# Optimization experiments

Measured on AMD Instinct MI355X. Metric: run time of the kernel, lower is better.

## Reference

```python
import jax, jax.numpy as jnp
import numpy as np

B, T = 64, 200
NUM_C2 = 2000
NUM_D = 1000
V = 128

# NOTE: Dropout layers are identity in eval mode; this reference implements eval-mode forward.

def setup_inputs() -> dict:
    key = jax.random.key(0)
    ks = jax.random.split(key, 19)
    s = 0.05
    def nrm(k, shape):
        return jax.random.normal(k, shape, jnp.float32) * s
    return {
        "c_seq": jax.random.randint(ks[0], (B, T), 0, NUM_C2),
        "d_seq": jax.random.randint(ks[1], (B, T), 0, NUM_D),
        "r_seq": (jax.random.uniform(ks[2], (B, T)) < 0.5).astype(jnp.float32),
        "D_emb": nrm(ks[3], (NUM_D, 1)),
        "v_d": nrm(ks[4], (V,)),
        "v_r": nrm(ks[5], (V,)),
        "v_c": nrm(ks[6], (V,)),
        "W_ih": nrm(ks[7], (3 * V, 2 * V)),
        "W_hh": nrm(ks[8], (3 * V, V)),
        "b_ih": nrm(ks[9], (3 * V,)),
        "b_hh": nrm(ks[10], (3 * V,)),
        "W1a": nrm(ks[11], (V, V)),
        "b1a": nrm(ks[12], (V,)),
        "W1b": nrm(ks[13], (1, V)),
        "b1b": nrm(ks[14], (1,)),
        "W2a": nrm(ks[15], (V, 3 * V)),
        "b2a": nrm(ks[16], (V,)),
        "W2b": nrm(ks[17], (1, V)),
        "b2b": nrm(ks[18], (1,)),
    }


def reference(c_seq, d_seq, r_seq, D_emb, v_d, v_r, v_c,
              W_ih, W_hh, b_ih, b_hh, W1a, b1a, W1b, b1b,
              W2a, b2a, W2b, b2b):
    gamma_seq = D_emb[d_seq]                 # [B,T,1]
    v_d_seq = gamma_seq * v_d                # [B,T,V]
    v_r_seq = r_seq[..., None] * v_r         # [B,T,V]
    x = jnp.concatenate([v_d_seq, v_r_seq], axis=-1)  # [B,T,2V]

    # --- GRU (PyTorch gate ordering r,z,n), h0 = 0 ---
    def gru_step(h, x_t):
        gi = x_t @ W_ih.T + b_ih
        gh = h @ W_hh.T + b_hh
        i_r, i_z, i_n = jnp.split(gi, 3, axis=-1)
        h_r, h_z, h_n = jnp.split(gh, 3, axis=-1)
        r = jax.nn.sigmoid(i_r + h_r)
        z = jax.nn.sigmoid(i_z + h_z)
        n = jnp.tanh(i_n + r * h_n)
        h_new = (1.0 - z) * n + z * h
        return h_new, h_new

    h0 = jnp.zeros((c_seq.shape[0], v_d.shape[0]), x.dtype)
    _, h_seq = jax.lax.scan(gru_step, h0, jnp.swapaxes(x, 0, 1))
    h_seq = jnp.swapaxes(h_seq, 0, 1)        # [B,T,V]

    # linear_1 (dropout = identity in eval)
    alpha_seq = (jax.nn.relu(h_seq @ W1a.T + b1a) @ W1b.T + b1b)[..., 0]  # [B,T]

    # --- sequential memory update over time ---
    def mem_step(C, inputs):
        c_t, vd_t, vr_t = inputs             # [B], [B,V], [B,V]
        beta = jnp.take_along_axis(C, c_t[:, None], axis=1)   # [B,1]
        vc = beta * v_c                       # [B,V]
        hh = jax.nn.relu(jnp.concatenate([vc, vd_t, vr_t], axis=-1) @ W2a.T + b2a)
        new_c = hh @ W2b.T + b2b              # [B,1]
        oh = jax.nn.one_hot(c_t, C.shape[1], dtype=C.dtype)   # [B,K]
        C_new = C * (1.0 - oh) + new_c * oh
        return C_new, C_new

    C0 = jnp.zeros((c_seq.shape[0], NUM_C2), x.dtype)
    _, C_seq = jax.lax.scan(
        mem_step, C0,
        (jnp.swapaxes(c_seq, 0, 1), jnp.swapaxes(v_d_seq, 0, 1), jnp.swapaxes(v_r_seq, 0, 1)))
    C_seq = jnp.swapaxes(C_seq, 0, 1)[..., None]   # [B,T,K,1]
    return alpha_seq, h_seq, C_seq
```

## Files before the change

### kernel.cpp

```cpp
#include <hip/hip_runtime.h>
#include <hip/hip_bf16.h>
#include <cstdint>

#define BB 64
#define TT 200
#define KN 2000
#define VV 128
#define NGRU 16

typedef __attribute__((ext_vector_type(8))) short bf16x8;
typedef __attribute__((ext_vector_type(4))) float f32x4;
typedef _Float16 half8 __attribute__((ext_vector_type(8)));


__device__ __forceinline__ float sigm(float x) {
    return __builtin_amdgcn_rcpf(1.f + __expf(-x));
}
__device__ __forceinline__ float tanh_f(float x) {
    float e = __expf(2.f * x);
    return 1.f - 2.f * __builtin_amdgcn_rcpf(e + 1.f);
}

__device__ __forceinline__ void soft_barrier() {
    asm volatile("s_waitcnt lgkmcnt(0)" ::: "memory");
    __builtin_amdgcn_s_barrier();
    __builtin_amdgcn_sched_barrier(0);
}

__global__ void pre_kernel(const float* __restrict__ v_d, const float* __restrict__ v_r,
                           const float* __restrict__ v_c, const float* __restrict__ W_ih,
                           const float* __restrict__ W2a, float* __restrict__ ws)
{
    int g = blockIdx.x * 256 + threadIdx.x;
    float* pd = ws;
    float* pr = ws + 384;
    float* uc = ws + 768;
    float* ud = ws + 896;
    float* ur = ws + 1024;
    if (g < 384) {
        float a = 0.f, b = 0.f;
        for (int k = 0; k < VV; ++k) {
            a = fmaf(W_ih[g * 256 + k], v_d[k], a);
            b = fmaf(W_ih[g * 256 + VV + k], v_r[k], b);
        }
        pd[g] = a; pr[g] = b;
    }
    if (g < VV) {
        float a = 0.f, b = 0.f, c = 0.f;
        for (int k = 0; k < VV; ++k) {
            a = fmaf(W2a[g * 384 + k], v_c[k], a);
            b = fmaf(W2a[g * 384 + VV + k], v_d[k], b);
            c = fmaf(W2a[g * 384 + 2 * VV + k], v_r[k], c);
        }
        uc[g] = a; ud[g] = b; ur[g] = c;
    }
}

__device__ __forceinline__ half8 load_cvt8h(const float* p) {
    float4 a = *(const float4*)p;
    float4 c = *(const float4*)(p + 4);
    half8 r;
    r[0] = (_Float16)a.x; r[1] = (_Float16)a.y; r[2] = (_Float16)a.z; r[3] = (_Float16)a.w;
    r[4] = (_Float16)c.x; r[5] = (_Float16)c.y; r[6] = (_Float16)c.z; r[7] = (_Float16)c.w;
    return r;
}

__global__ __launch_bounds__(512, 1) void fused_kernel(
    const int* __restrict__ c_seq, const int* __restrict__ d_seq,
    const float* __restrict__ r_seq, const float* __restrict__ D_emb,
    const float* __restrict__ Whh, const float* __restrict__ bih,
    const float* __restrict__ bhh, const float* __restrict__ W2b,
    const float* __restrict__ b2a, const float* __restrict__ b2b,
    const float* __restrict__ ws, float* __restrict__ C_out,
    float* __restrict__ h_out)
{
    __shared__ __align__(16) _Float16 H_half[16 * 136];
    __shared__ __align__(8) float gam4[TT * 4], r4[TT * 4];
    __shared__ __align__(16) float C[KN];
    __shared__ float gam_row[TT], r_row[TT], n_row[TT];
    __shared__ int c_row[TT + 1];

    int tid = threadIdx.x;

    if (blockIdx.x < NGRU) {
        int b0 = blockIdx.x * 4;
        const float* pd = ws;
        const float* pr = ws + 384;

        for (int i = tid; i < TT * 4; i += 512) {
            int t = i >> 2, rr = i & 3;
            gam4[i] = D_emb[d_seq[(b0 + rr) * TT + t]];
            r4[i] = r_seq[(b0 + rr) * TT + t];
        }
        for (int i = tid; i < 16 * 136; i += 512) H_half[i] = (_Float16)0.f;

        int wid = tid >> 6, l = tid & 63;
        int cl = l & 15, gq = l >> 4;
        int nn = wid * 16 + cl;

        const float* wr = Whh + (size_t)nn * VV + gq * 8;
        const float* wz = Whh + (size_t)(nn + 128) * VV + gq * 8;
        const float* wn = Whh + (size_t)(nn + 256) * VV + gq * 8;
        half8 br0 = load_cvt8h(wr),      br1 = load_cvt8h(wr + 32),
              br2 = load_cvt8h(wr + 64), br3 = load_cvt8h(wr + 96);
        half8 bz0 = load_cvt8h(wz),      bz1 = load_cvt8h(wz + 32),
              bz2 = load_cvt8h(wz + 64), bz3 = load_cvt8h(wz + 96);
        half8 bn0 = load_cvt8h(wn),      bn1 = load_cvt8h(wn + 32),
              bn2 = load_cvt8h(wn + 64), bn3 = load_cvt8h(wn + 96);

        float gr_pd = pd[nn],        gr_pr = pr[nn],        gr_b = bih[nn] + bhh[nn];
        float gz_pd = pd[nn + 128],  gz_pr = pr[nn + 128],  gz_b = bih[nn + 128] + bhh[nn + 128];
        float gn_pd = pd[nn + 256],  gn_pr = pr[nn + 256],  gn_b = bih[nn + 256];
        float gn_bh = bhh[nn + 256];

        float h0 = 0.f;
        __syncthreads();

        for (int t = 0; t < TT; ++t) {
            asm volatile("" : "+v"(br0), "+v"(br1), "+v"(br2), "+v"(br3),
                              "+v"(bz0), "+v"(bz1), "+v"(bz2), "+v"(bz3),
                              "+v"(bn0), "+v"(bn1), "+v"(bn2), "+v"(bn3));
            const int ab = cl * 136 + gq * 8;
            half8 a0 = *(const half8*)&H_half[ab];
            half8 a1 = *(const half8*)&H_half[ab + 32];
            half8 a2 = *(const half8*)&H_half[ab + 64];
            half8 a3 = *(const half8*)&H_half[ab + 96];
            float g1 = gam4[t * 4 + gq];
            float q1 = r4[t * 4 + gq];

            f32x4 accr = {0.f, 0.f, 0.f, 0.f};
            f32x4 accz = {0.f, 0.f, 0.f, 0.f};
            f32x4 accn = {0.f, 0.f, 0.f, 0.f};
            accr[0] = fmaf(g1, gr_pd, fmaf(q1, gr_pr, gr_b));
            accz[0] = fmaf(g1, gz_pd, fmaf(q1, gz_pr, gz_b));
            accn[0] = gn_bh;
            float gin0 = fmaf(g1, gn_pd, fmaf(q1, gn_pr, gn_b));

            accr = __builtin_amdgcn_mfma_f32_16x16x32_f16(a0, br0, accr, 0, 0, 0);
            accr = __builtin_amdgcn_mfma_f32_16x16x32_f16(a1, br1, accr, 0, 0, 0);
            accr = __builtin_amdgcn_mfma_f32_16x16x32_f16(a2, br2, accr, 0, 0, 0);
            accr = __builtin_amdgcn_mfma_f32_16x16x32_f16(a3, br3, accr, 0, 0, 0);
            accz = __builtin_amdgcn_mfma_f32_16x16x32_f16(a0, bz0, accz, 0, 0, 0);
            accz = __builtin_amdgcn_mfma_f32_16x16x32_f16(a1, bz1, accz, 0, 0, 0);
            accz = __builtin_amdgcn_mfma_f32_16x16x32_f16(a2, bz2, accz, 0, 0, 0);
            accz = __builtin_amdgcn_mfma_f32_16x16x32_f16(a3, bz3, accz, 0, 0, 0);
            accn = __builtin_amdgcn_mfma_f32_16x16x32_f16(a0, bn0, accn, 0, 0, 0);
            accn = __builtin_amdgcn_mfma_f32_16x16x32_f16(a1, bn1, accn, 0, 0, 0);
            accn = __builtin_amdgcn_mfma_f32_16x16x32_f16(a2, bn2, accn, 0, 0, 0);
            accn = __builtin_amdgcn_mfma_f32_16x16x32_f16(a3, bn3, accn, 0, 0, 0);

            {
                float rg0 = sigm(accr[0]);
                float zg0 = sigm(accz[0]);
                float ng0 = tanh_f(fmaf(rg0, accn[0], gin0));
                h0 = fmaf(1.f - zg0, ng0, zg0 * h0);
                h_out[((size_t)(b0 + gq) * TT + t) * VV + nn] = h0;
                H_half[(gq * 4) * 136 + nn] = (_Float16)h0;
            }
            soft_barrier();
        }
    } else {
        int b = blockIdx.x - NGRU;
        const float* uc = ws + 768;
        const float* ud = ws + 896;
        const float* ur = ws + 1024;
        for (int i = tid; i < KN; i += 512) C[i] = 0.f;
        if (tid < TT) {
            gam_row[tid] = D_emb[d_seq[b * TT + tid]];
            r_row[tid] = r_seq[b * TT + tid];
            c_row[tid] = c_seq[b * TT + tid];
        }
        if (tid == 0) c_row[TT] = 0;
        __syncthreads();

        if (tid < 64) {
            int l = tid;
            float uc0 = uc[l], uc1 = uc[l + 64];
            float ud0 = ud[l], ud1 = ud[l + 64];
            float ur0 = ur[l], ur1 = ur[l + 64];
            float ba0 = b2a[l], ba1 = b2a[l + 64];
            float wb0 = W2b[l], wb1 = W2b[l + 64];
            float bb = b2b[0];
            float beta = 0.f;
            int ct = c_row[0];
            for (int t = 0; t < TT; ++t) {
                int ct1 = c_row[t + 1];
                float cpref = C[ct1];
                float g = gam_row[t], rr = r_row[t];
                float hh0 = fmaxf(fmaf(beta, uc0, fmaf(g, ud0, fmaf(rr, ur0, ba0))), 0.f);
                float hh1 = fmaxf(fmaf(beta, uc1, fmaf(g, ud1, fmaf(rr, ur1, ba1))), 0.f);
                float p = fmaf(hh0, wb0, hh1 * wb1);
                #pragma unroll
                for (int m = 32; m > 0; m >>= 1) p += __shfl_xor(p, m);
                float nc = p + bb;
                if (l == 0) { C[ct] = nc; n_row[t] = nc; }
                beta = (ct1 == ct) ? nc : cpref;
                ct = ct1;
            }
        }
        __syncthreads();

        int k0 = tid * 4;
        if (k0 < KN) {
            float4 cur = {0.f, 0.f, 0.f, 0.f};
            float* cop = C_out + (size_t)b * TT * KN + k0;
            for (int t = 0; t < TT; ++t) {
                int c = c_row[t];
                unsigned d = (unsigned)(c - k0);
                if (d < 4u) {
                    float v = n_row[t];
                    cur.x = (d == 0u) ? v : cur.x;
                    cur.y = (d == 1u) ? v : cur.y;
                    cur.z = (d == 2u) ? v : cur.z;
                    cur.w = (d == 3u) ? v : cur.w;
                }
                *(float4*)(cop + (size_t)t * KN) = cur;
            }
        }
    }
}

__device__ __forceinline__ short f2bf(float f) {
    uint32_t u = __float_as_uint(f);
    u = (u + 0x7FFFu + ((u >> 16) & 1u)) >> 16;
    return (short)u;
}
__device__ __forceinline__ bf16x8 load_cvt8(const float* p) {
    float4 a = *(const float4*)p;
    float4 c = *(const float4*)(p + 4);
    bf16x8 r;
    r[0] = f2bf(a.x); r[1] = f2bf(a.y); r[2] = f2bf(a.z); r[3] = f2bf(a.w);
    r[4] = f2bf(c.x); r[5] = f2bf(c.y); r[6] = f2bf(c.z); r[7] = f2bf(c.w);
    return r;
}

__global__ __launch_bounds__(512) void alpha_kernel(
    const float* __restrict__ h_seq, const float* __restrict__ W1a,
    const float* __restrict__ b1a, const float* __restrict__ W1b,
    const float* __restrict__ b1b, float* __restrict__ alpha)
{
    __shared__ __align__(16) short W1s[128 * 136];
    __shared__ float b1s[128], w1bs[128];
    int tid = threadIdx.x;
    for (int i = tid * 8; i < 128 * 128; i += 512 * 8) {
        int row = i >> 7, col = i & 127;
        *(bf16x8*)&W1s[row * 136 + col] = load_cvt8(W1a + i);
    }
    if (tid < 128) { b1s[tid] = b1a[tid]; w1bs[tid] = W1b[tid]; }
    __syncthreads();

    int wave = tid >> 6, lane = tid & 63;
    int tile = blockIdx.x * 8 + wave;
    int rowbase = tile * 16;
    int rl = lane & 15, g = lane >> 4;
    const float* hp = h_seq + (size_t)(rowbase + rl) * VV + g * 8;
    bf16x8 a0 = load_cvt8(hp);
    bf16x8 a1 = load_cvt8(hp + 32);
    bf16x8 a2 = load_cvt8(hp + 64);
    bf16x8 a3 = load_cvt8(hp + 96);
    float p0 = 0.f, p1 = 0.f, p2 = 0.f, p3 = 0.f;
    float bb = b1b[0];
    #pragma unroll
    for (int jt = 0; jt < 8; ++jt) {
        int j = jt * 16 + rl;
        const short* wp = &W1s[j * 136 + g * 8];
        f32x4 acc = {0.f, 0.f, 0.f, 0.f};
        acc = __builtin_amdgcn_mfma_f32_16x16x32_bf16(a0, *(const bf16x8*)wp, acc, 0, 0, 0);
        acc = __builtin_amdgcn_mfma_f32_16x16x32_bf16(a1, *(const bf16x8*)(wp + 32), acc, 0, 0, 0);
        acc = __builtin_amdgcn_mfma_f32_16x16x32_bf16(a2, *(const bf16x8*)(wp + 64), acc, 0, 0, 0);
        acc = __builtin_amdgcn_mfma_f32_16x16x32_bf16(a3, *(const bf16x8*)(wp + 96), acc, 0, 0, 0);
        float bj = b1s[j], wj = w1bs[j];
        p0 += fmaxf(acc[0] + bj, 0.f) * wj;
        p1 += fmaxf(acc[1] + bj, 0.f) * wj;
        p2 += fmaxf(acc[2] + bj, 0.f) * wj;
        p3 += fmaxf(acc[3] + bj, 0.f) * wj;
    }
    #pragma unroll
    for (int m = 1; m < 16; m <<= 1) {
        p0 += __shfl_xor(p0, m);
        p1 += __shfl_xor(p1, m);
        p2 += __shfl_xor(p2, m);
        p3 += __shfl_xor(p3, m);
    }
    if (rl == 0) {
        alpha[rowbase + g * 4 + 0] = p0 + bb;
        alpha[rowbase + g * 4 + 1] = p1 + bb;
        alpha[rowbase + g * 4 + 2] = p2 + bb;
        alpha[rowbase + g * 4 + 3] = p3 + bb;
    }
}

extern "C" void kernel_launch(void* const* d_in, const int* in_sizes, int n_in,
                              void* d_out, int out_size, void* d_ws, size_t ws_size,
                              hipStream_t stream)
{
    const int*   c_seq = (const int*)d_in[0];
    const int*   d_seq = (const int*)d_in[1];
    const float* r_seq = (const float*)d_in[2];
    const float* D_emb = (const float*)d_in[3];
    const float* v_d   = (const float*)d_in[4];
    const float* v_r   = (const float*)d_in[5];
    const float* v_c   = (const float*)d_in[6];
    const float* W_ih  = (const float*)d_in[7];
    const float* W_hh  = (const float*)d_in[8];
    const float* b_ih  = (const float*)d_in[9];
    const float* b_hh  = (const float*)d_in[10];
    const float* W1a   = (const float*)d_in[11];
    const float* b1a   = (const float*)d_in[12];
    const float* W1b   = (const float*)d_in[13];
    const float* b1b   = (const float*)d_in[14];
    const float* W2a   = (const float*)d_in[15];
    const float* b2a   = (const float*)d_in[16];
    const float* W2b   = (const float*)d_in[17];
    const float* b2b   = (const float*)d_in[18];

    float* out   = (float*)d_out;
    float* alpha = out;
    float* h_seq = out + 12800;
    float* C_out = out + 12800 + 1638400;
    float* ws    = (float*)d_ws;

    hipLaunchKernelGGL(pre_kernel, dim3(2), dim3(256), 0, stream,
                       v_d, v_r, v_c, W_ih, W2a, ws);
    hipLaunchKernelGGL(fused_kernel, dim3(NGRU + BB), dim3(512), 0, stream,
                       c_seq, d_seq, r_seq, D_emb, W_hh, b_ih, b_hh,
                       W2b, b2a, b2b, ws, C_out, h_seq);
    hipLaunchKernelGGL(alpha_kernel, dim3(100), dim3(512), 0, stream,
                       h_seq, W1a, b1a, W1b, b1b, alpha);
}
```

Before: 116.4 us.

## Process two independent batch groups per GRU block with split-K MFMA chains

Measured after the change: 175.2 us. +50.5%, slower.

```diff
diff --git a/kernel.cpp b/kernel.cpp
--- a/kernel.cpp
+++ b/kernel.cpp
@@ -6,7 +6,7 @@
 #define TT 200
 #define KN 2000
 #define VV 128
-#define NGRU 16
+#define NGRU 8
 
 typedef __attribute__((ext_vector_type(8))) short bf16x8;
 typedef __attribute__((ext_vector_type(4))) float f32x4;
@@ -74,8 +74,8 @@
     const float* __restrict__ ws, float* __restrict__ C_out,
     float* __restrict__ h_out)
 {
-    __shared__ __align__(16) _Float16 H_half[16 * 136];
-    __shared__ __align__(8) float gam4[TT * 4], r4[TT * 4];
+    __shared__ __align__(16) _Float16 H_half[2][16 * 136];
+    __shared__ __align__(8) float gam4[2][TT * 4], r4[2][TT * 4];
     __shared__ __align__(16) float C[KN];
     __shared__ float gam_row[TT], r_row[TT], n_row[TT];
     __shared__ int c_row[TT + 1];
@@ -83,16 +83,18 @@
     int tid = threadIdx.x;
 
     if (blockIdx.x < NGRU) {
-        int b0 = blockIdx.x * 4;
+        int bB = blockIdx.x * 8;
         const float* pd = ws;
         const float* pr = ws + 384;
 
-        for (int i = tid; i < TT * 4; i += 512) {
-            int t = i >> 2, rr = i & 3;
-            gam4[i] = D_emb[d_seq[(b0 + rr) * TT + t]];
-            r4[i] = r_seq[(b0 + rr) * TT + t];
-        }
-        for (int i = tid; i < 16 * 136; i += 512) H_half[i] = (_Float16)0.f;
+        for (int i = tid; i < TT * 8; i += 512) {
+            int t = i >> 3, rr = i & 7;
+            int grp = rr >> 2, r = rr & 3;
+            gam4[grp][t * 4 + r] = D_emb[d_seq[(bB + rr) * TT + t]];
+            r4[grp][t * 4 + r] = r_seq[(bB + rr) * TT + t];
+        }
+        for (int i = tid; i < 2 * 16 * 136; i += 512)
+            ((_Float16*)H_half)[i] = (_Float16)0.f;
 
         int wid = tid >> 6, l = tid & 63;
         int cl = l & 15, gq = l >> 4;
@@ -113,49 +115,78 @@
         float gn_pd = pd[nn + 256],  gn_pr = pr[nn + 256],  gn_b = bih[nn + 256];
         float gn_bh = bhh[nn + 256];
 
-        float h0 = 0.f;
+        float hA = 0.f, hB = 0.f;
         __syncthreads();
+
+        float* hpA = h_out + ((size_t)(bB + gq) * TT) * VV + nn;
+        float* hpB = h_out + ((size_t)(bB + 4 + gq) * TT) * VV + nn;
 
         for (int t = 0; t < TT; ++t) {
             asm volatile("" : "+v"(br0), "+v"(br1), "+v"(br2), "+v"(br3),
                               "+v"(bz0), "+v"(bz1), "+v"(bz2), "+v"(bz3),
                               "+v"(bn0), "+v"(bn1), "+v"(bn2), "+v"(bn3));
             const int ab = cl * 136 + gq * 8;
-            half8 a0 = *(const half8*)&H_half[ab];
-            half8 a1 = *(const half8*)&H_half[ab + 32];
-            half8 a2 = *(const half8*)&H_half[ab + 64];
-            half8 a3 = *(const half8*)&H_half[ab + 96];
-            float g1 = gam4[t * 4 + gq];
-            float q1 = r4[t * 4 + gq];
-
-            f32x4 accr = {0.f, 0.f, 0.f, 0.f};
-            f32x4 accz = {0.f, 0.f, 0.f, 0.f};
-            f32x4 accn = {0.f, 0.f, 0.f, 0.f};
-            accr[0] = fmaf(g1, gr_pd, fmaf(q1, gr_pr, gr_b));
-            accz[0] = fmaf(g1, gz_pd, fmaf(q1, gz_pr, gz_b));
-            accn[0] = gn_bh;
-            float gin0 = fmaf(g1, gn_pd, fmaf(q1, gn_pr, gn_b));
-
-            accr = __builtin_amdgcn_mfma_f32_16x16x32_f16(a0, br0, accr, 0, 0, 0);
-            accr = __builtin_amdgcn_mfma_f32_16x16x32_f16(a1, br1, accr, 0, 0, 0);
-            accr = __builtin_amdgcn_mfma_f32_16x16x32_f16(a2, br2, accr, 0, 0, 0);
-            accr = __builtin_amdgcn_mfma_f32_16x16x32_f16(a3, br3, accr, 0, 0, 0);
-            accz = __builtin_amdgcn_mfma_f32_16x16x32_f16(a0, bz0, accz, 0, 0, 0);
-            accz = __builtin_amdgcn_mfma_f32_16x16x32_f16(a1, bz1, accz, 0, 0, 0);
-            accz = __builtin_amdgcn_mfma_f32_16x16x32_f16(a2, bz2, accz, 0, 0, 0);
-            accz = __builtin_amdgcn_mfma_f32_16x16x32_f16(a3, bz3, accz, 0, 0, 0);
-            accn = __builtin_amdgcn_mfma_f32_16x16x32_f16(a0, bn0, accn, 0, 0, 0);
-            accn = __builtin_amdgcn_mfma_f32_16x16x32_f16(a1, bn1, accn, 0, 0, 0);
-            accn = __builtin_amdgcn_mfma_f32_16x16x32_f16(a2, bn2, accn, 0, 0, 0);
-            accn = __builtin_amdgcn_mfma_f32_16x16x32_f16(a3, bn3, accn, 0, 0, 0);
+            half8 aA0 = *(const half8*)&H_half[0][ab];
+            half8 aA1 = *(const half8*)&H_half[0][ab + 32];
+            half8 aA2 = *(const half8*)&H_half[0][ab + 64];
+            half8 aA3 = *(const half8*)&H_half[0][ab + 96];
+            half8 aB0 = *(const half8*)&H_half[1][ab];
+            half8 aB1 = *(const half8*)&H_half[1][ab + 32];
+            half8 aB2 = *(const half8*)&H_half[1][ab + 64];
+            half8 aB3 = *(const half8*)&H_half[1][ab + 96];
+            float g1A = gam4[0][t * 4 + gq], q1A = r4[0][t * 4 + gq];
+            float g1B = gam4[1][t * 4 + gq], q1B = r4[1][t * 4 + gq];
+
+            f32x4 z4 = {0.f, 0.f, 0.f, 0.f};
+            f32x4 rAl = z4, rAh = z4, zAl = z4, zAh = z4, nAl = z4, nAh = z4;
+            f32x4 rBl = z4, rBh = z4, zBl = z4, zBh = z4, nBl = z4, nBh = z4;
+            rAl[0] = fmaf(g1A, gr_pd, fmaf(q1A, gr_pr, gr_b));
+            zAl[0] = fmaf(g1A, gz_pd, fmaf(q1A, gz_pr, gz_b));
+            nAl[0] = gn_bh;
+            float ginA = fmaf(g1A, gn_pd, fmaf(q1A, gn_pr, gn_b));
+            rBl[0] = fmaf(g1B, gr_pd, fmaf(q1B, gr_pr, gr_b));
+            zBl[0] = fmaf(g1B, gz_pd, fmaf(q1B, gz_pr, gz_b));
+            nBl[0] = gn_bh;
+            float ginB = fmaf(g1B, gn_pd, fmaf(q1B, gn_pr, gn_b));
+
+            rAl = __builtin_amdgcn_mfma_f32_16x16x32_f16(aA0, br0, rAl, 0, 0, 0);
+            rBl = __builtin_amdgcn_mfma_f32_16x16x32_f16(aB0, br0, rBl, 0, 0, 0);
+            rAh = __builtin_amdgcn_mfma_f32_16x16x32_f16(aA2, br2, rAh, 0, 0, 0);
+            rBh = __builtin_amdgcn_mfma_f32_16x16x32_f16(aB2, br2, rBh, 0, 0, 0);
+            rAl = __builtin_amdgcn_mfma_f32_16x16x32_f16(aA1, br1, rAl, 0, 0, 0);
+            rBl = __builtin_amdgcn_mfma_f32_16x16x32_f16(aB1, br1, rBl, 0, 0, 0);
+            rAh = __builtin_amdgcn_mfma_f32_16x16x32_f16(aA3, br3, rAh, 0, 0, 0);
+            rBh = __builtin_amdgcn_mfma_f32_16x16x32_f16(aB3, br3, rBh, 0, 0, 0);
+            zAl = __builtin_amdgcn_mfma_f32_16x16x32_f16(aA0, bz0, zAl, 0, 0, 0);
+            zBl = __builtin_amdgcn_mfma_f32_16x16x32_f16(aB0, bz0, zBl, 0, 0, 0);
+            zAh = __builtin_amdgcn_mfma_f32_16x16x32_f16(aA2, bz2, zAh, 0, 0, 0);
+            zBh = __builtin_amdgcn_mfma_f32_16x16x32_f16(aB2, bz2, zBh, 0, 0, 0);
+            zAl = __builtin_amdgcn_mfma_f32_16x16x32_f16(aA1, bz1, zAl, 0, 0, 0);
+            zBl = __builtin_amdgcn_mfma_f32_16x16x32_f16(aB1, bz1, zBl, 0, 0, 0);
+            zAh = __builtin_amdgcn_mfma_f32_16x16x32_f16(aA3, bz3, zAh, 0, 0, 0);
+            zBh = __builtin_amdgcn_mfma_f32_16x16x32_f16(aB3, bz3, zBh, 0, 0, 0);
+            nAl = __builtin_amdgcn_mfma_f32_16x16x32_f16(aA0, bn0, nAl, 0, 0, 0);
+            nBl = __builtin_amdgcn_mfma_f32_16x16x32_f16(aB0, bn0, nBl, 0, 0, 0);
+            nAh = __builtin_amdgcn_mfma_f32_16x16x32_f16(aA2, bn2, nAh, 0, 0, 0);
+            nBh = __builtin_amdgcn_mfma_f32_16x16x32_f16(aB2, bn2, nBh, 0, 0, 0);
+            nAl = __builtin_amdgcn_mfma_f32_16x16x32_f16(aA1, bn1, nAl, 0, 0, 0);
+            nBl = __builtin_amdgcn_mfma_f32_16x16x32_f16(aB1, bn1, nBl, 0, 0, 0);
+            nAh = __builtin_amdgcn_mfma_f32_16x16x32_f16(aA3, bn3, nAh, 0, 0, 0);
+            nBh = __builtin_amdgcn_mfma_f32_16x16x32_f16(aB3, bn3, nBh, 0, 0, 0);
 
             {
-                float rg0 = sigm(accr[0]);
-                float zg0 = sigm(accz[0]);
-                float ng0 = tanh_f(fmaf(rg0, accn[0], gin0));
-                h0 = fmaf(1.f - zg0, ng0, zg0 * h0);
-                h_out[((size_t)(b0 + gq) * TT + t) * VV + nn] = h0;
-                H_half[(gq * 4) * 136 + nn] = (_Float16)h0;
+                float rgA = sigm(rAl[0] + rAh[0]);
+                float rgB = sigm(rBl[0] + rBh[0]);
+                float zgA = sigm(zAl[0] + zAh[0]);
+                float zgB = sigm(zBl[0] + zBh[0]);
+                float ngA = tanh_f(fmaf(rgA, nAl[0] + nAh[0], ginA));
+                float ngB = tanh_f(fmaf(rgB, nBl[0] + nBh[0], ginB));
+                hA = fmaf(1.f - zgA, ngA, zgA * hA);
+                hB = fmaf(1.f - zgB, ngB, zgB * hB);
+                hpA[t * VV] = hA;
+                hpB[t * VV] = hB;
+                H_half[0][(gq * 4) * 136 + nn] = (_Float16)hA;
+                H_half[1][(gq * 4) * 136 + nn] = (_Float16)hB;
             }
             soft_barrier();
         }
```
